# Kernel optimization log

Measured on AMD Instinct MI355X. Metric: run time of the kernel, lower is better.

The kernel has to match this reference:

```python
import jax, jax.numpy as jnp
import numpy as np

B, S, D = 2, 2048, 1024
H = 16
HD = D // H  # head_dim = 64
NEG = -1e30  # finite stand-in for -inf; masked entries are zeroed after softmax so math matches


def setup_inputs() -> dict:
    key = jax.random.key(0)
    ks = jax.random.split(key, 10)
    q = jax.random.normal(ks[0], (B, S, D), dtype=jnp.float32)
    k = jax.random.normal(ks[1], (B, S, D), dtype=jnp.float32)
    v = jax.random.normal(ks[2], (B, S, D), dtype=jnp.float32)
    mask = jax.random.randint(ks[3], (B, S), 0, 2).astype(bool)
    s = 1.0 / np.sqrt(D)
    Wq = jax.random.uniform(ks[4], (D, D), jnp.float32, -s, s)
    bq = jax.random.uniform(ks[5], (D,), jnp.float32, -s, s)
    Wk = jax.random.uniform(ks[6], (D, D), jnp.float32, -s, s)
    bk = jax.random.uniform(ks[7], (D,), jnp.float32, -s, s)
    Wv = jax.random.uniform(ks[8], (D, D), jnp.float32, -s, s)
    bv = jax.random.uniform(ks[9], (D,), jnp.float32, -s, s)
    return {"q": q, "k": k, "v": v, "mask": mask,
            "Wq": Wq, "bq": bq, "Wk": Wk, "bk": bk, "Wv": Wv, "bv": bv}


def _split_heads(x):
    # [B,S,D] -> [H,B,S,HD]  (matches permute(2,0,1,3) in torch)
    return x.reshape(B, S, H, HD).transpose(2, 0, 1, 3)


def reference(q, k, v, mask, Wq, bq, Wk, bk, Wv, bv):
    mq = _split_heads(q @ Wq.T + bq)
    mk = _split_heads(k @ Wk.T + bk)
    mv = _split_heads(v @ Wv.T + bv)
    # scores: [H,B,Sq,Sk]
    scores = jnp.einsum('hbqd,hbkd->hbqk', mq, mk) / jnp.sqrt(jnp.float32(HD))
    pair_mask = (mask[:, :, None] & mask[:, None, :])[None]  # [1,B,S,S]
    scores = jnp.where(pair_mask, scores, NEG)
    attn = jax.nn.softmax(scores, axis=-1)
    attn = jnp.where(pair_mask, attn, 0.0)
    out = jnp.einsum('hbqk,hbkd->hbqd', attn, mv)
    # [H,B,S,HD] -> [B,S,D]
    return out.transpose(1, 2, 0, 3).reshape(B, S, H * HD)
```

## Files before the change

kernel.cpp:

```cpp
#include <hip/hip_runtime.h>
#include <math.h>

#define B_ 2
#define S_ 2048
#define D_ 1024
#define H_ 16
#define HD_ 64
#define LOG2E 1.44269504088896340736f

typedef __bf16 bf16_t;
typedef bf16_t bf16x8 __attribute__((ext_vector_type(8)));
typedef bf16_t bf16x4v __attribute__((ext_vector_type(4)));
typedef float f32x4 __attribute__((ext_vector_type(4)));

#define GLOBAL_LOAD_LDS16(gp, lp)                                              \
    __builtin_amdgcn_global_load_lds(                                          \
        (const __attribute__((address_space(1))) void*)(gp),                   \
        (__attribute__((address_space(3))) void*)(lp), 16, 0, 0)

__global__ __launch_bounds__(256) void cvt_kernel(
    const float* __restrict__ q, const float* __restrict__ k,
    const float* __restrict__ v, const float* __restrict__ wq,
    const float* __restrict__ wk, const float* __restrict__ wv,
    const int* __restrict__ msk,
    bf16_t* __restrict__ qb, bf16_t* __restrict__ kb, bf16_t* __restrict__ vb,
    bf16_t* __restrict__ wqb, bf16_t* __restrict__ wkb, bf16_t* __restrict__ wvb,
    float* __restrict__ kbias)
{
    const size_t NT = (size_t)1 << 20;
    const size_t NW = (size_t)1 << 18;
    size_t g = (size_t)blockIdx.x * 256 + threadIdx.x;

    const float* src;
    bf16_t* dst;
    size_t off;
    if (g < 3 * NT) {
        int t = (int)(g >> 20);
        off = (g & (NT - 1)) * 4;
        src = (t == 0) ? q : (t == 1) ? k : v;
        dst = (t == 0) ? qb : (t == 1) ? kb : vb;
    } else if (g < 3 * NT + 3 * NW) {
        size_t gw = g - 3 * NT;
        int t = (int)(gw >> 18);
        off = (gw & (NW - 1)) * 4;
        src = (t == 0) ? wq : (t == 1) ? wk : wv;
        dst = (t == 0) ? wqb : (t == 1) ? wkb : wvb;
    } else {
        size_t gm = g - (3 * NT + 3 * NW);
        if (gm >= (size_t)B_ * S_ / 4) return;
        size_t idx = gm * 4;
        int4 mi = *(const int4*)(msk + idx);
        float4 o4;
        const float VB = -8.0f * LOG2E;
        const float MB = -1.44269504e30f;
        o4.x = mi.x ? VB : MB;
        o4.y = mi.y ? VB : MB;
        o4.z = mi.z ? VB : MB;
        o4.w = mi.w ? VB : MB;
        *(float4*)(kbias + idx) = o4;
        return;
    }

    float4 f = *(const float4*)(src + off);
    bf16x4v o;
    o[0] = (bf16_t)f.x; o[1] = (bf16_t)f.y;
    o[2] = (bf16_t)f.z; o[3] = (bf16_t)f.w;
    *(bf16x4v*)(dst + off) = o;
}

__global__ __launch_bounds__(256) void proj_mfma(
    const bf16_t* __restrict__ X0, const bf16_t* __restrict__ X1,
    const bf16_t* __restrict__ X2, const bf16_t* __restrict__ W0,
    const bf16_t* __restrict__ W1, const bf16_t* __restrict__ W2,
    const float* __restrict__ b0, const float* __restrict__ b1,
    const float* __restrict__ b2, bf16_t* __restrict__ o0,
    bf16_t* __restrict__ o1, bf16_t* __restrict__ o2)
{
    __shared__ __align__(16) bf16_t As[128 * 32];
    __shared__ __align__(16) bf16_t Bs[128 * 32];

    const int z = blockIdx.z;
    const bf16_t* X = (z == 0) ? X0 : (z == 1) ? X1 : X2;
    const bf16_t* W = (z == 0) ? W0 : (z == 1) ? W1 : W2;
    const float* bias = (z == 0) ? b0 : (z == 1) ? b1 : b2;
    bf16_t* out = (z == 0) ? o0 : (z == 1) ? o1 : o2;
    const float oscale = (z == 0) ? (0.125f * LOG2E) : 1.0f;

    const int tid  = threadIdx.x;
    const int w    = tid >> 6;
    const int lane = tid & 63;
    const int L    = lane & 15;
    const int quad = lane >> 4;
    const int wr   = (w >> 1) * 64;
    const int wc   = (w & 1) * 64;
    const int row0 = blockIdx.x * 128;
    const int col0 = blockIdx.y * 128;

    const int lr = lane >> 2;
    const int lc = (lane & 3) * 8;

    f32x4 acc[4][4];
    #pragma unroll
    for (int i = 0; i < 4; ++i)
        #pragma unroll
        for (int j = 0; j < 4; ++j) {
            acc[i][j][0] = 0.f; acc[i][j][1] = 0.f;
            acc[i][j][2] = 0.f; acc[i][j][3] = 0.f;
        }

    for (int k0 = 0; k0 < D_; k0 += 32) {
        __syncthreads();
        #pragma unroll
        for (int i = 0; i < 2; ++i) {
            const int rA = i * 64 + w * 16;
            GLOBAL_LOAD_LDS16(X + (size_t)(row0 + rA + lr) * D_ + k0 + lc,
                              &As[rA * 32]);
            GLOBAL_LOAD_LDS16(W + (size_t)(col0 + rA + lr) * D_ + k0 + lc,
                              &Bs[rA * 32]);
        }
        __syncthreads();

        bf16x8 aF[4], bF[4];
        #pragma unroll
        for (int t = 0; t < 4; ++t) {
            aF[t] = *(const bf16x8*)&As[(wr + t * 16 + L) * 32 + quad * 8];
            bF[t] = *(const bf16x8*)&Bs[(wc + t * 16 + L) * 32 + quad * 8];
        }
        #pragma unroll
        for (int mt = 0; mt < 4; ++mt)
            #pragma unroll
            for (int nt = 0; nt < 4; ++nt)
                acc[mt][nt] = __builtin_amdgcn_mfma_f32_16x16x32_bf16(
                    aF[mt], bF[nt], acc[mt][nt], 0, 0, 0);
    }

    if (z == 2) {
        #pragma unroll
        for (int nt = 0; nt < 4; ++nt) {
            const int j  = col0 + wc + nt * 16 + L;
            const float bval = bias[j];
            const int h  = j >> 6;
            const int hd = j & 63;
            #pragma unroll
            for (int mt = 0; mt < 4; ++mt) {
                const int n0 = row0 + wr + mt * 16 + quad * 4;
                const int b  = n0 >> 11;
                const int s  = n0 & (S_ - 1);
                bf16x4v p;
                #pragma unroll
                for (int r = 0; r < 4; ++r)
                    p[r] = (bf16_t)(acc[mt][nt][r] + bval);
                *(bf16x4v*)(out + ((size_t)(b * H_ + h) * HD_ + hd) * S_ + s) = p;
            }
        }
    } else {
        #pragma unroll
        for (int nt = 0; nt < 4; ++nt) {
            const int j  = col0 + wc + nt * 16 + L;
            const float bval = bias[j];
            const int h  = j >> 6;
            const int hd = j & 63;
            #pragma unroll
            for (int mt = 0; mt < 4; ++mt)
                #pragma unroll
                for (int r = 0; r < 4; ++r) {
                    const int n = row0 + wr + mt * 16 + quad * 4 + r;
                    const int b = n >> 11;
                    const int s = n & (S_ - 1);
                    out[((((size_t)b * H_ + h) * S_ + s) * HD_) + hd] =
                        (bf16_t)((acc[mt][nt][r] + bval) * oscale);
                }
        }
    }
}

__global__ __launch_bounds__(256) void attn_kernel(
    const bf16_t* __restrict__ Q, const bf16_t* __restrict__ K,
    const bf16_t* __restrict__ Vt, const float* __restrict__ kbias,
    const int* __restrict__ mask, float* __restrict__ out)
{
    constexpr int LD = 72;
    __shared__ bf16_t Ks[64 * LD];
    __shared__ bf16_t Vs[64 * LD];
    __shared__ bf16_t Pt[4][32 * LD];

    const int tid  = threadIdx.x;
    const int w    = tid >> 6;
    const int lane = tid & 63;
    const int L    = lane & 15;
    const int quad = lane >> 4;
    const int h    = blockIdx.y;
    const int b    = blockIdx.z;
    const int bh   = b * H_ + h;
    const int q0   = blockIdx.x * 128;

    const bf16_t* kbase = K  + (size_t)bh * S_ * HD_;
    const bf16_t* vbase = Vt + (size_t)bh * HD_ * S_;
    const float*  bbase = kbias + b * S_;
    const int*    mrow  = mask + b * S_;

    const int sr = tid >> 3;
    const int sc2 = (tid & 7) * 8;

    bf16x8 aQ[2][2];
    #pragma unroll
    for (int qb = 0; qb < 2; ++qb) {
        const bf16_t* qp = Q + ((size_t)bh * S_ + q0 + w * 32 + qb * 16 + L) * HD_;
        aQ[qb][0] = *(const bf16x8*)(qp + quad * 8);
        aQ[qb][1] = *(const bf16x8*)(qp + 32 + quad * 8);
    }

    f32x4 o[2][4];
    #pragma unroll
    for (int qb = 0; qb < 2; ++qb)
        #pragma unroll
        for (int f = 0; f < 4; ++f) {
            o[qb][f][0]=0.f; o[qb][f][1]=0.f; o[qb][f][2]=0.f; o[qb][f][3]=0.f;
        }
    float l_[2] = {0.f, 0.f};

    bf16x8 kr0, kr1, vr0, vr1;
    f32x4  bias_n[4];
    {
        kr0 = *(const bf16x8*)(kbase + (size_t)sr * HD_ + sc2);
        kr1 = *(const bf16x8*)(kbase + (size_t)(sr + 32) * HD_ + sc2);
        vr0 = *(const bf16x8*)(vbase + (size_t)sr * S_ + sc2);
        vr1 = *(const bf16x8*)(vbase + (size_t)(sr + 32) * S_ + sc2);
        #pragma unroll
        for (int f = 0; f < 4; ++f)
            bias_n[f] = *(const f32x4*)(bbase + f * 16 + quad * 4);
    }

    #pragma unroll 2
    for (int kt = 0; kt < S_; kt += 64) {
        __syncthreads();
        *(bf16x8*)&Ks[sr * LD + sc2]        = kr0;
        *(bf16x8*)&Ks[(sr + 32) * LD + sc2] = kr1;
        *(bf16x8*)&Vs[sr * LD + sc2]        = vr0;
        *(bf16x8*)&Vs[(sr + 32) * LD + sc2] = vr1;
        f32x4 bias_c[4];
        #pragma unroll
        for (int f = 0; f < 4; ++f) bias_c[f] = bias_n[f];
        __syncthreads();

        if (kt + 64 < S_) {
            const int kn = kt + 64;
            kr0 = *(const bf16x8*)(kbase + (size_t)(kn + sr) * HD_ + sc2);
            kr1 = *(const bf16x8*)(kbase + (size_t)(kn + sr + 32) * HD_ + sc2);
            vr0 = *(const bf16x8*)(vbase + (size_t)sr * S_ + kn + sc2);
            vr1 = *(const bf16x8*)(vbase + (size_t)(sr + 32) * S_ + kn + sc2);
            #pragma unroll
            for (int f = 0; f < 4; ++f)
                bias_n[f] = *(const f32x4*)(bbase + kn + f * 16 + quad * 4);
        }

        bf16x8 aK[4][2];
        #pragma unroll
        for (int f = 0; f < 4; ++f) {
            aK[f][0] = *(const bf16x8*)&Ks[(f * 16 + L) * LD + quad * 8];
            aK[f][1] = *(const bf16x8*)&Ks[(f * 16 + L) * LD + 32 + quad * 8];
        }

        bf16_t* pw = &Pt[w][0];
        #pragma unroll
        for (int qb = 0; qb < 2; ++qb) {
            #pragma unroll
            for (int f = 0; f < 4; ++f) {
                f32x4 z = bias_c[f];
                __builtin_amdgcn_s_setprio(1);
                z = __builtin_amdgcn_mfma_f32_16x16x32_bf16(aK[f][0], aQ[qb][0], z, 0, 0, 0);
                z = __builtin_amdgcn_mfma_f32_16x16x32_bf16(aK[f][1], aQ[qb][1], z, 0, 0, 0);
                __builtin_amdgcn_s_setprio(0);
                float e0 = exp2f(z[0]);
                float e1 = exp2f(z[1]);
                float e2 = exp2f(z[2]);
                float e3 = exp2f(z[3]);
                l_[qb] += (e0 + e1) + (e2 + e3);
                bf16x4v p4;
                p4[0] = (bf16_t)e0; p4[1] = (bf16_t)e1;
                p4[2] = (bf16_t)e2; p4[3] = (bf16_t)e3;
                *(bf16x4v*)&pw[(qb * 16 + L) * LD + f * 16 + quad * 4] = p4;
            }
        }

        bf16x8 aP[2][2];
        #pragma unroll
        for (int qb = 0; qb < 2; ++qb) {
            aP[qb][0] = *(const bf16x8*)&pw[(qb * 16 + L) * LD + quad * 8];
            aP[qb][1] = *(const bf16x8*)&pw[(qb * 16 + L) * LD + 32 + quad * 8];
        }

        __builtin_amdgcn_s_setprio(1);
        #pragma unroll
        for (int f = 0; f < 4; ++f) {
            bf16x8 bV0 = *(const bf16x8*)&Vs[(f * 16 + L) * LD + quad * 8];
            bf16x8 bV1 = *(const bf16x8*)&Vs[(f * 16 + L) * LD + 32 + quad * 8];
            #pragma unroll
            for (int qb = 0; qb < 2; ++qb) {
                o[qb][f] = __builtin_amdgcn_mfma_f32_16x16x32_bf16(aP[qb][0], bV0, o[qb][f], 0, 0, 0);
                o[qb][f] = __builtin_amdgcn_mfma_f32_16x16x32_bf16(aP[qb][1], bV1, o[qb][f], 0, 0, 0);
            }
        }
        __builtin_amdgcn_s_setprio(0);
    }

    #pragma unroll
    for (int qb = 0; qb < 2; ++qb) {
        float t = l_[qb];
        t += __shfl_xor(t, 16);
        t += __shfl_xor(t, 32);
        int qv = mrow[q0 + w * 32 + qb * 16 + L];
        l_[qb] = (qv && t > 0.f) ? (1.0f / t) : 0.0f;
    }

    #pragma unroll
    for (int qb = 0; qb < 2; ++qb) {
        float inv[4];
        #pragma unroll
        for (int r = 0; r < 4; ++r)
            inv[r] = __shfl(l_[qb], quad * 4 + r);
        float* obase = out + ((size_t)b * S_ + q0 + w * 32 + qb * 16 + quad * 4) * D_ + h * HD_;
        #pragma unroll
        for (int f = 0; f < 4; ++f)
            #pragma unroll
            for (int r = 0; r < 4; ++r)
                obase[r * D_ + f * 16 + L] = o[qb][f][r] * inv[r];
    }
}

extern "C" void kernel_launch(void* const* d_in, const int* in_sizes, int n_in,
                              void* d_out, int out_size, void* d_ws, size_t ws_size,
                              hipStream_t stream)
{
    const float* q    = (const float*)d_in[0];
    const float* k    = (const float*)d_in[1];
    const float* v    = (const float*)d_in[2];
    const int*   mask = (const int*)d_in[3];
    const float* Wq   = (const float*)d_in[4];
    const float* bq   = (const float*)d_in[5];
    const float* Wk   = (const float*)d_in[6];
    const float* bk   = (const float*)d_in[7];
    const float* Wv   = (const float*)d_in[8];
    const float* bv   = (const float*)d_in[9];
    float* out = (float*)d_out;

    const size_t PE = (size_t)B_ * S_ * D_;
    const size_t WE = (size_t)D_ * D_;

    bf16_t* qb    = (bf16_t*)d_ws;
    bf16_t* kb    = qb + PE;
    bf16_t* vb    = kb + PE;
    bf16_t* wqb   = vb + PE;
    bf16_t* wkb   = wqb + WE;
    bf16_t* wvb   = wkb + WE;
    bf16_t* mq    = wvb + WE;
    bf16_t* mk    = mq + PE;
    bf16_t* vt    = mk + PE;
    float*  kbias = (float*)(vt + PE);

    const size_t ngroups = 3 * (PE / 4) + 3 * (WE / 4) + (size_t)B_ * S_ / 4;
    dim3 cgrid((ngroups + 255) / 256);
    cvt_kernel<<<cgrid, 256, 0, stream>>>(q, k, v, Wq, Wk, Wv, mask,
                                          qb, kb, vb, wqb, wkb, wvb, kbias);

    dim3 pgrid(4096 / 128, 1024 / 128, 3);
    proj_mfma<<<pgrid, 256, 0, stream>>>(qb, kb, vb, wqb, wkb, wvb,
                                         bq, bk, bv, mq, mk, vt);

    dim3 agrid(S_ / 128, H_, B_);
    attn_kernel<<<agrid, 256, 0, stream>>>(mq, mk, vt, kbias, mask, out);
}
```

Before: 226.4 us.

## Halve attention query tile, remap blocks across XCDs, compute row sums via MFMA

```diff
diff --git a/kernel.cpp b/kernel.cpp
--- a/kernel.cpp
+++ b/kernel.cpp
@@ -182,17 +182,20 @@
     constexpr int LD = 72;
     __shared__ bf16_t Ks[64 * LD];
     __shared__ bf16_t Vs[64 * LD];
-    __shared__ bf16_t Pt[4][32 * LD];
+    __shared__ bf16_t Pt[4][16 * LD];
 
     const int tid  = threadIdx.x;
     const int w    = tid >> 6;
     const int lane = tid & 63;
     const int L    = lane & 15;
     const int quad = lane >> 4;
-    const int h    = blockIdx.y;
-    const int b    = blockIdx.z;
+
+    const int orig = blockIdx.x + 32 * (blockIdx.y + 16 * blockIdx.z);
+    const int work = (orig & 7) * 128 + (orig >> 3);
+    const int q0   = (work & 31) * 64;
+    const int h    = (work >> 5) & 15;
+    const int b    = work >> 9;
     const int bh   = b * H_ + h;
-    const int q0   = blockIdx.x * 128;
 
     const bf16_t* kbase = K  + (size_t)bh * S_ * HD_;
     const bf16_t* vbase = Vt + (size_t)bh * HD_ * S_;
@@ -202,22 +205,24 @@
     const int sr = tid >> 3;
     const int sc2 = (tid & 7) * 8;
 
-    bf16x8 aQ[2][2];
+    bf16x8 aQ[2];
+    {
+        const bf16_t* qp = Q + ((size_t)bh * S_ + q0 + w * 16 + L) * HD_;
+        aQ[0] = *(const bf16x8*)(qp + quad * 8);
+        aQ[1] = *(const bf16x8*)(qp + 32 + quad * 8);
+    }
+
+    f32x4 o[4];
     #pragma unroll
-    for (int qb = 0; qb < 2; ++qb) {
-        const bf16_t* qp = Q + ((size_t)bh * S_ + q0 + w * 32 + qb * 16 + L) * HD_;
-        aQ[qb][0] = *(const bf16x8*)(qp + quad * 8);
-        aQ[qb][1] = *(const bf16x8*)(qp + 32 + quad * 8);
-    }
-
-    f32x4 o[2][4];
+    for (int f = 0; f < 4; ++f) {
+        o[f][0]=0.f; o[f][1]=0.f; o[f][2]=0.f; o[f][3]=0.f;
+    }
+    f32x4 ol;
+    ol[0]=0.f; ol[1]=0.f; ol[2]=0.f; ol[3]=0.f;
+
+    bf16x8 ones;
     #pragma unroll
-    for (int qb = 0; qb < 2; ++qb)
-        #pragma unroll
-        for (int f = 0; f < 4; ++f) {
-            o[qb][f][0]=0.f; o[qb][f][1]=0.f; o[qb][f][2]=0.f; o[qb][f][3]=0.f;
-        }
-    float l_[2] = {0.f, 0.f};
+    for (int i = 0; i < 8; ++i) ones[i] = (bf16_t)1.0f;
 
     bf16x8 kr0, kr1, vr0, vr1;
     f32x4  bias_n[4];
@@ -231,7 +236,6 @@
             bias_n[f] = *(const f32x4*)(bbase + f * 16 + quad * 4);
     }
 
-    #pragma unroll 2
     for (int kt = 0; kt < S_; kt += 64) {
         __syncthreads();
         *(bf16x8*)&Ks[sr * LD + sc2]        = kr0;
@@ -263,69 +267,45 @@
 
         bf16_t* pw = &Pt[w][0];
         #pragma unroll
-        for (int qb = 0; qb < 2; ++qb) {
-            #pragma unroll
-            for (int f = 0; f < 4; ++f) {
-                f32x4 z = bias_c[f];
-                __builtin_amdgcn_s_setprio(1);
-                z = __builtin_amdgcn_mfma_f32_16x16x32_bf16(aK[f][0], aQ[qb][0], z, 0, 0, 0);
-                z = __builtin_amdgcn_mfma_f32_16x16x32_bf16(aK[f][1], aQ[qb][1], z, 0, 0, 0);
-                __builtin_amdgcn_s_setprio(0);
-                float e0 = exp2f(z[0]);
-                float e1 = exp2f(z[1]);
-                float e2 = exp2f(z[2]);
-                float e3 = exp2f(z[3]);
-                l_[qb] += (e0 + e1) + (e2 + e3);
-                bf16x4v p4;
-                p4[0] = (bf16_t)e0; p4[1] = (bf16_t)e1;
-                p4[2] = (bf16_t)e2; p4[3] = (bf16_t)e3;
-                *(bf16x4v*)&pw[(qb * 16 + L) * LD + f * 16 + quad * 4] = p4;
-            }
-        }
-
-        bf16x8 aP[2][2];
-        #pragma unroll
-        for (int qb = 0; qb < 2; ++qb) {
-            aP[qb][0] = *(const bf16x8*)&pw[(qb * 16 + L) * LD + quad * 8];
-            aP[qb][1] = *(const bf16x8*)&pw[(qb * 16 + L) * LD + 32 + quad * 8];
-        }
-
-        __builtin_amdgcn_s_setprio(1);
+        for (int f = 0; f < 4; ++f) {
+            f32x4 z = bias_c[f];
+            z = __builtin_amdgcn_mfma_f32_16x16x32_bf16(aK[f][0], aQ[0], z, 0, 0, 0);
+            z = __builtin_amdgcn_mfma_f32_16x16x32_bf16(aK[f][1], aQ[1], z, 0, 0, 0);
+            bf16x4v p4;
+            p4[0] = (bf16_t)exp2f(z[0]);
+            p4[1] = (bf16_t)exp2f(z[1]);
+            p4[2] = (bf16_t)exp2f(z[2]);
+            p4[3] = (bf16_t)exp2f(z[3]);
+            *(bf16x4v*)&pw[L * LD + f * 16 + quad * 4] = p4;
+        }
+
+        bf16x8 aP0 = *(const bf16x8*)&pw[L * LD + quad * 8];
+        bf16x8 aP1 = *(const bf16x8*)&pw[L * LD + 32 + quad * 8];
+
         #pragma unroll
         for (int f = 0; f < 4; ++f) {
             bf16x8 bV0 = *(const bf16x8*)&Vs[(f * 16 + L) * LD + quad * 8];
             bf16x8 bV1 = *(const bf16x8*)&Vs[(f * 16 + L) * LD + 32 + quad * 8];
-            #pragma unroll
-            for (int qb = 0; qb < 2; ++qb) {
-                o[qb][f] = __builtin_amdgcn_mfma_f32_16x16x32_bf16(aP[qb][0], bV0, o[qb][f], 0, 0, 0);
-                o[qb][f] = __builtin_amdgcn_mfma_f32_16x16x32_bf16(aP[qb][1], bV1, o[qb][f], 0, 0, 0);
-            }
-        }
-        __builtin_amdgcn_s_setprio(0);
-    }
-
+            o[f] = __builtin_amdgcn_mfma_f32_16x16x32_bf16(aP0, bV0, o[f], 0, 0, 0);
+            o[f] = __builtin_amdgcn_mfma_f32_16x16x32_bf16(aP1, bV1, o[f], 0, 0, 0);
+        }
+        ol = __builtin_amdgcn_mfma_f32_16x16x32_bf16(aP0, ones, ol, 0, 0, 0);
+        ol = __builtin_amdgcn_mfma_f32_16x16x32_bf16(aP1, ones, ol, 0, 0, 0);
+    }
+
+    const int4 m4 = *(const int4*)&mrow[q0 + w * 16 + quad * 4];
+    float inv[4];
+    inv[0] = (m4.x && ol[0] > 0.f) ? (1.0f / ol[0]) : 0.0f;
+    inv[1] = (m4.y && ol[1] > 0.f) ? (1.0f / ol[1]) : 0.0f;
+    inv[2] = (m4.z && ol[2] > 0.f) ? (1.0f / ol[2]) : 0.0f;
+    inv[3] = (m4.w && ol[3] > 0.f) ? (1.0f / ol[3]) : 0.0f;
+
+    float* obase = out + ((size_t)b * S_ + q0 + w * 16 + quad * 4) * D_ + h * HD_;
     #pragma unroll
-    for (int qb = 0; qb < 2; ++qb) {
-        float t = l_[qb];
-        t += __shfl_xor(t, 16);
-        t += __shfl_xor(t, 32);
-        int qv = mrow[q0 + w * 32 + qb * 16 + L];
-        l_[qb] = (qv && t > 0.f) ? (1.0f / t) : 0.0f;
-    }
-
-    #pragma unroll
-    for (int qb = 0; qb < 2; ++qb) {
-        float inv[4];
+    for (int f = 0; f < 4; ++f)
         #pragma unroll
         for (int r = 0; r < 4; ++r)
-            inv[r] = __shfl(l_[qb], quad * 4 + r);
-        float* obase = out + ((size_t)b * S_ + q0 + w * 32 + qb * 16 + quad * 4) * D_ + h * HD_;
-        #pragma unroll
-        for (int f = 0; f < 4; ++f)
-            #pragma unroll
-            for (int r = 0; r < 4; ++r)
-                obase[r * D_ + f * 16 + L] = o[qb][f][r] * inv[r];
-    }
+            obase[r * D_ + f * 16 + L] = o[f][r] * inv[r];
 }
 
 extern "C" void kernel_launch(void* const* d_in, const int* in_sizes, int n_in,
@@ -367,6 +347,6 @@
     proj_mfma<<<pgrid, 256, 0, stream>>>(qb, kb, vb, wqb, wkb, wvb,
                                          bq, bk, bv, mq, mk, vt);
 
-    dim3 agrid(S_ / 128, H_, B_);
+    dim3 agrid(S_ / 64, H_, B_);
     attn_kernel<<<agrid, 256, 0, stream>>>(mq, mk, vt, kbias, mask, out);
 }
```

New measurement: 239.8 us. 5.9% more time.

## Double-buffer LDS in projection and attention, swizzle LDS, remap blocks, MFMA row sums

Applied to the files above, without the earlier changes.

```diff
diff --git a/kernel.cpp b/kernel.cpp
--- a/kernel.cpp
+++ b/kernel.cpp
@@ -76,10 +76,15 @@
     const float* __restrict__ b2, bf16_t* __restrict__ o0,
     bf16_t* __restrict__ o1, bf16_t* __restrict__ o2)
 {
-    __shared__ __align__(16) bf16_t As[128 * 32];
-    __shared__ __align__(16) bf16_t Bs[128 * 32];
-
-    const int z = blockIdx.z;
+    __shared__ __align__(16) bf16_t As[2][128 * 32];
+    __shared__ __align__(16) bf16_t Bs[2][128 * 32];
+
+    const int orig = blockIdx.x + 32 * blockIdx.y + 256 * blockIdx.z;
+    const int work = (orig & 7) * 96 + (orig >> 3);
+    const int bx = work & 31;
+    const int by = (work >> 5) & 7;
+    const int z  = work >> 8;
+
     const bf16_t* X = (z == 0) ? X0 : (z == 1) ? X1 : X2;
     const bf16_t* W = (z == 0) ? W0 : (z == 1) ? W1 : W2;
     const float* bias = (z == 0) ? b0 : (z == 1) ? b1 : b2;
@@ -93,8 +98,8 @@
     const int quad = lane >> 4;
     const int wr   = (w >> 1) * 64;
     const int wc   = (w & 1) * 64;
-    const int row0 = blockIdx.x * 128;
-    const int col0 = blockIdx.y * 128;
+    const int row0 = bx * 128;
+    const int col0 = by * 128;
 
     const int lr = lane >> 2;
     const int lc = (lane & 3) * 8;
@@ -108,23 +113,33 @@
             acc[i][j][2] = 0.f; acc[i][j][3] = 0.f;
         }
 
-    for (int k0 = 0; k0 < D_; k0 += 32) {
-        __syncthreads();
-        #pragma unroll
-        for (int i = 0; i < 2; ++i) {
-            const int rA = i * 64 + w * 16;
-            GLOBAL_LOAD_LDS16(X + (size_t)(row0 + rA + lr) * D_ + k0 + lc,
-                              &As[rA * 32]);
-            GLOBAL_LOAD_LDS16(W + (size_t)(col0 + rA + lr) * D_ + k0 + lc,
-                              &Bs[rA * 32]);
-        }
-        __syncthreads();
+    #pragma unroll
+    for (int i = 0; i < 2; ++i) {
+        const int rA = i * 64 + w * 16;
+        GLOBAL_LOAD_LDS16(X + (size_t)(row0 + rA + lr) * D_ + lc, &As[0][rA * 32]);
+        GLOBAL_LOAD_LDS16(W + (size_t)(col0 + rA + lr) * D_ + lc, &Bs[0][rA * 32]);
+    }
+    __syncthreads();
+
+    for (int kk = 0; kk < 32; ++kk) {
+        const int cur = kk & 1;
+        if (kk < 31) {
+            const int k0 = (kk + 1) * 32;
+            #pragma unroll
+            for (int i = 0; i < 2; ++i) {
+                const int rA = i * 64 + w * 16;
+                GLOBAL_LOAD_LDS16(X + (size_t)(row0 + rA + lr) * D_ + k0 + lc,
+                                  &As[cur ^ 1][rA * 32]);
+                GLOBAL_LOAD_LDS16(W + (size_t)(col0 + rA + lr) * D_ + k0 + lc,
+                                  &Bs[cur ^ 1][rA * 32]);
+            }
+        }
 
         bf16x8 aF[4], bF[4];
         #pragma unroll
         for (int t = 0; t < 4; ++t) {
-            aF[t] = *(const bf16x8*)&As[(wr + t * 16 + L) * 32 + quad * 8];
-            bF[t] = *(const bf16x8*)&Bs[(wc + t * 16 + L) * 32 + quad * 8];
+            aF[t] = *(const bf16x8*)&As[cur][(wr + t * 16 + L) * 32 + quad * 8];
+            bF[t] = *(const bf16x8*)&Bs[cur][(wc + t * 16 + L) * 32 + quad * 8];
         }
         #pragma unroll
         for (int mt = 0; mt < 4; ++mt)
@@ -132,6 +147,8 @@
             for (int nt = 0; nt < 4; ++nt)
                 acc[mt][nt] = __builtin_amdgcn_mfma_f32_16x16x32_bf16(
                     aF[mt], bF[nt], acc[mt][nt], 0, 0, 0);
+
+        __syncthreads();
     }
 
     if (z == 2) {
@@ -179,28 +196,35 @@
     const bf16_t* __restrict__ Vt, const float* __restrict__ kbias,
     const int* __restrict__ mask, float* __restrict__ out)
 {
-    constexpr int LD = 72;
-    __shared__ bf16_t Ks[64 * LD];
-    __shared__ bf16_t Vs[64 * LD];
-    __shared__ bf16_t Pt[4][32 * LD];
+    __shared__ bf16_t Ks[2][64 * 64];
+    __shared__ bf16_t Vs[2][64 * 64];
+    __shared__ bf16_t Pt[4][32 * 64];
 
     const int tid  = threadIdx.x;
     const int w    = tid >> 6;
     const int lane = tid & 63;
     const int L    = lane & 15;
     const int quad = lane >> 4;
-    const int h    = blockIdx.y;
-    const int b    = blockIdx.z;
+    const int L7   = L & 7;
+
+    const int orig = blockIdx.x + 16 * (blockIdx.y + 16 * blockIdx.z);
+    const int work = (orig & 7) * 64 + (orig >> 3);
+    const int q0   = (work & 15) * 128;
+    const int h    = (work >> 4) & 15;
+    const int b    = work >> 8;
     const int bh   = b * H_ + h;
-    const int q0   = blockIdx.x * 128;
 
     const bf16_t* kbase = K  + (size_t)bh * S_ * HD_;
     const bf16_t* vbase = Vt + (size_t)bh * HD_ * S_;
     const float*  bbase = kbias + b * S_;
     const int*    mrow  = mask + b * S_;
 
-    const int sr = tid >> 3;
-    const int sc2 = (tid & 7) * 8;
+    const int sr  = tid >> 3;
+    const int c8  = tid & 7;
+    const int sc2 = c8 * 8;
+    const int swz = ((c8 ^ (sr & 7)) * 8);
+    const int st0 = sr * 64 + swz;
+    const int st1 = (sr + 32) * 64 + swz;
 
     bf16x8 aQ[2][2];
     #pragma unroll
@@ -217,108 +241,131 @@
         for (int f = 0; f < 4; ++f) {
             o[qb][f][0]=0.f; o[qb][f][1]=0.f; o[qb][f][2]=0.f; o[qb][f][3]=0.f;
         }
-    float l_[2] = {0.f, 0.f};
+    f32x4 ol[2];
+    #pragma unroll
+    for (int qb = 0; qb < 2; ++qb) {
+        ol[qb][0]=0.f; ol[qb][1]=0.f; ol[qb][2]=0.f; ol[qb][3]=0.f;
+    }
+
+    bf16x8 ones;
+    #pragma unroll
+    for (int i = 0; i < 8; ++i) ones[i] = (bf16_t)1.0f;
 
     bf16x8 kr0, kr1, vr0, vr1;
-    f32x4  bias_n[4];
-    {
-        kr0 = *(const bf16x8*)(kbase + (size_t)sr * HD_ + sc2);
-        kr1 = *(const bf16x8*)(kbase + (size_t)(sr + 32) * HD_ + sc2);
-        vr0 = *(const bf16x8*)(vbase + (size_t)sr * S_ + sc2);
-        vr1 = *(const bf16x8*)(vbase + (size_t)(sr + 32) * S_ + sc2);
-        #pragma unroll
-        for (int f = 0; f < 4; ++f)
-            bias_n[f] = *(const f32x4*)(bbase + f * 16 + quad * 4);
-    }
-
-    #pragma unroll 2
-    for (int kt = 0; kt < S_; kt += 64) {
-        __syncthreads();
-        *(bf16x8*)&Ks[sr * LD + sc2]        = kr0;
-        *(bf16x8*)&Ks[(sr + 32) * LD + sc2] = kr1;
-        *(bf16x8*)&Vs[sr * LD + sc2]        = vr0;
-        *(bf16x8*)&Vs[(sr + 32) * LD + sc2] = vr1;
-        f32x4 bias_c[4];
-        #pragma unroll
-        for (int f = 0; f < 4; ++f) bias_c[f] = bias_n[f];
-        __syncthreads();
-
-        if (kt + 64 < S_) {
-            const int kn = kt + 64;
+    f32x4  bias_c[4], bias_n[4];
+    kr0 = *(const bf16x8*)(kbase + (size_t)sr * HD_ + sc2);
+    kr1 = *(const bf16x8*)(kbase + (size_t)(sr + 32) * HD_ + sc2);
+    vr0 = *(const bf16x8*)(vbase + (size_t)sr * S_ + sc2);
+    vr1 = *(const bf16x8*)(vbase + (size_t)(sr + 32) * S_ + sc2);
+    #pragma unroll
+    for (int f = 0; f < 4; ++f)
+        bias_c[f] = *(const f32x4*)(bbase + f * 16 + quad * 4);
+
+    *(bf16x8*)&Ks[0][st0] = kr0;
+    *(bf16x8*)&Ks[0][st1] = kr1;
+    *(bf16x8*)&Vs[0][st0] = vr0;
+    *(bf16x8*)&Vs[0][st1] = vr1;
+
+    kr0 = *(const bf16x8*)(kbase + (size_t)(64 + sr) * HD_ + sc2);
+    kr1 = *(const bf16x8*)(kbase + (size_t)(64 + sr + 32) * HD_ + sc2);
+    vr0 = *(const bf16x8*)(vbase + (size_t)sr * S_ + 64 + sc2);
+    vr1 = *(const bf16x8*)(vbase + (size_t)(sr + 32) * S_ + 64 + sc2);
+    #pragma unroll
+    for (int f = 0; f < 4; ++f)
+        bias_n[f] = *(const f32x4*)(bbase + 64 + f * 16 + quad * 4);
+
+    __syncthreads();
+
+    for (int t = 0; t < 32; ++t) {
+        const int cur = t & 1;
+        bf16_t* ks  = &Ks[cur][0];
+        bf16_t* vs  = &Vs[cur][0];
+
+        if (t < 31) {
+            bf16_t* ksn = &Ks[cur ^ 1][0];
+            bf16_t* vsn = &Vs[cur ^ 1][0];
+            *(bf16x8*)&ksn[st0] = kr0;
+            *(bf16x8*)&ksn[st1] = kr1;
+            *(bf16x8*)&vsn[st0] = vr0;
+            *(bf16x8*)&vsn[st1] = vr1;
+        }
+        if (t < 30) {
+            const int kn = (t + 2) * 64;
             kr0 = *(const bf16x8*)(kbase + (size_t)(kn + sr) * HD_ + sc2);
             kr1 = *(const bf16x8*)(kbase + (size_t)(kn + sr + 32) * HD_ + sc2);
             vr0 = *(const bf16x8*)(vbase + (size_t)sr * S_ + kn + sc2);
             vr1 = *(const bf16x8*)(vbase + (size_t)(sr + 32) * S_ + kn + sc2);
+        }
+
+        bf16x8 aK[4][2];
+        #pragma unroll
+        for (int f = 0; f < 4; ++f) {
+            const int row = (f * 16 + L) * 64;
+            aK[f][0] = *(const bf16x8*)&ks[row + ((quad ^ L7) * 8)];
+            aK[f][1] = *(const bf16x8*)&ks[row + (((4 | quad) ^ L7) * 8)];
+        }
+
+        bf16_t* pw = &Pt[w][0];
+        #pragma unroll
+        for (int qb = 0; qb < 2; ++qb) {
+            const int prow = (qb * 16 + L) * 64;
+            #pragma unroll
+            for (int f = 0; f < 4; ++f) {
+                f32x4 z = bias_c[f];
+                z = __builtin_amdgcn_mfma_f32_16x16x32_bf16(aK[f][0], aQ[qb][0], z, 0, 0, 0);
+                z = __builtin_amdgcn_mfma_f32_16x16x32_bf16(aK[f][1], aQ[qb][1], z, 0, 0, 0);
+                bf16x4v p4;
+                p4[0] = (bf16_t)exp2f(z[0]);
+                p4[1] = (bf16_t)exp2f(z[1]);
+                p4[2] = (bf16_t)exp2f(z[2]);
+                p4[3] = (bf16_t)exp2f(z[3]);
+                *(bf16x4v*)&pw[prow + (((f * 2 + (quad >> 1)) ^ L7) * 8) + (quad & 1) * 4] = p4;
+            }
+        }
+
+        #pragma unroll
+        for (int f = 0; f < 4; ++f) bias_c[f] = bias_n[f];
+        if (t < 30) {
+            const int kn = (t + 2) * 64;
             #pragma unroll
             for (int f = 0; f < 4; ++f)
                 bias_n[f] = *(const f32x4*)(bbase + kn + f * 16 + quad * 4);
         }
 
-        bf16x8 aK[4][2];
+        bf16x8 aP[2][2];
+        #pragma unroll
+        for (int qb = 0; qb < 2; ++qb) {
+            const int prow = (qb * 16 + L) * 64;
+            aP[qb][0] = *(const bf16x8*)&pw[prow + ((quad ^ L7) * 8)];
+            aP[qb][1] = *(const bf16x8*)&pw[prow + (((4 | quad) ^ L7) * 8)];
+            ol[qb] = __builtin_amdgcn_mfma_f32_16x16x32_bf16(aP[qb][0], ones, ol[qb], 0, 0, 0);
+            ol[qb] = __builtin_amdgcn_mfma_f32_16x16x32_bf16(aP[qb][1], ones, ol[qb], 0, 0, 0);
+        }
+
         #pragma unroll
         for (int f = 0; f < 4; ++f) {
-            aK[f][0] = *(const bf16x8*)&Ks[(f * 16 + L) * LD + quad * 8];
-            aK[f][1] = *(const bf16x8*)&Ks[(f * 16 + L) * LD + 32 + quad * 8];
-        }
-
-        bf16_t* pw = &Pt[w][0];
-        #pragma unroll
-        for (int qb = 0; qb < 2; ++qb) {
-            #pragma unroll
-            for (int f = 0; f < 4; ++f) {
-                f32x4 z = bias_c[f];
-                __builtin_amdgcn_s_setprio(1);
-                z = __builtin_amdgcn_mfma_f32_16x16x32_bf16(aK[f][0], aQ[qb][0], z, 0, 0, 0);
-                z = __builtin_amdgcn_mfma_f32_16x16x32_bf16(aK[f][1], aQ[qb][1], z, 0, 0, 0);
-                __builtin_amdgcn_s_setprio(0);
-                float e0 = exp2f(z[0]);
-                float e1 = exp2f(z[1]);
-                float e2 = exp2f(z[2]);
-                float e3 = exp2f(z[3]);
-                l_[qb] += (e0 + e1) + (e2 + e3);
-                bf16x4v p4;
-                p4[0] = (bf16_t)e0; p4[1] = (bf16_t)e1;
-                p4[2] = (bf16_t)e2; p4[3] = (bf16_t)e3;
-                *(bf16x4v*)&pw[(qb * 16 + L) * LD + f * 16 + quad * 4] = p4;
-            }
-        }
-
-        bf16x8 aP[2][2];
-        #pragma unroll
-        for (int qb = 0; qb < 2; ++qb) {
-            aP[qb][0] = *(const bf16x8*)&pw[(qb * 16 + L) * LD + quad * 8];
-            aP[qb][1] = *(const bf16x8*)&pw[(qb * 16 + L) * LD + 32 + quad * 8];
-        }
-
-        __builtin_amdgcn_s_setprio(1);
-        #pragma unroll
-        for (int f = 0; f < 4; ++f) {
-            bf16x8 bV0 = *(const bf16x8*)&Vs[(f * 16 + L) * LD + quad * 8];
-            bf16x8 bV1 = *(const bf16x8*)&Vs[(f * 16 + L) * LD + 32 + quad * 8];
+            const int row = (f * 16 + L) * 64;
+            bf16x8 bV0 = *(const bf16x8*)&vs[row + ((quad ^ L7) * 8)];
+            bf16x8 bV1 = *(const bf16x8*)&vs[row + (((4 | quad) ^ L7) * 8)];
             #pragma unroll
             for (int qb = 0; qb < 2; ++qb) {
                 o[qb][f] = __builtin_amdgcn_mfma_f32_16x16x32_bf16(aP[qb][0], bV0, o[qb][f], 0, 0, 0);
                 o[qb][f] = __builtin_amdgcn_mfma_f32_16x16x32_bf16(aP[qb][1], bV1, o[qb][f], 0, 0, 0);
             }
         }
-        __builtin_amdgcn_s_setprio(0);
+
+        __syncthreads();
     }
 
     #pragma unroll
     for (int qb = 0; qb < 2; ++qb) {
-        float t = l_[qb];
-        t += __shfl_xor(t, 16);
-        t += __shfl_xor(t, 32);
-        int qv = mrow[q0 + w * 32 + qb * 16 + L];
-        l_[qb] = (qv && t > 0.f) ? (1.0f / t) : 0.0f;
-    }
-
-    #pragma unroll
-    for (int qb = 0; qb < 2; ++qb) {
+        const int4 m4 = *(const int4*)&mrow[q0 + w * 32 + qb * 16 + quad * 4];
         float inv[4];
-        #pragma unroll
-        for (int r = 0; r < 4; ++r)
-            inv[r] = __shfl(l_[qb], quad * 4 + r);
+        inv[0] = (m4.x && ol[qb][0] > 0.f) ? (1.0f / ol[qb][0]) : 0.0f;
+        inv[1] = (m4.y && ol[qb][1] > 0.f) ? (1.0f / ol[qb][1]) : 0.0f;
+        inv[2] = (m4.z && ol[qb][2] > 0.f) ? (1.0f / ol[qb][2]) : 0.0f;
+        inv[3] = (m4.w && ol[qb][3] > 0.f) ? (1.0f / ol[qb][3]) : 0.0f;
+
         float* obase = out + ((size_t)b * S_ + q0 + w * 32 + qb * 16 + quad * 4) * D_ + h * HD_;
         #pragma unroll
         for (int f = 0; f < 4; ++f)
```

Result: slower. 232.9 us (+2.8%).
